# Kernel optimization log

Measured on AMD Instinct MI355X. Metric: run time of the kernel, lower is better.

Reference implementation:

```python
import jax, jax.numpy as jnp
import numpy as np

B, L, D, P = 8, 2048, 1024, 4  # batch, length, word_dim, phrase_len


def setup_inputs() -> dict:
    key = jax.random.key(0)
    kx, kw, kb = jax.random.split(key, 3)
    x = jax.random.normal(kx, (B, L, D), dtype=jnp.float32)
    # torch nn.Linear(phrase_dim, word_dim): W [out=D, in=D*P], b [D]
    scale = 1.0 / np.sqrt(D * P)
    W = jax.random.uniform(kw, (D, D * P), dtype=jnp.float32, minval=-scale, maxval=scale)
    b = jax.random.uniform(kb, (D,), dtype=jnp.float32, minval=-scale, maxval=scale)
    return {"x": x, "W": W, "b": b}


def reference(x, W, b):
    Bs, Ls, Ds = x.shape
    Ps = W.shape[1] // Ds  # phrase_len
    # gram[i][:, t] = x[:, t - i] (zero for t < i): left-pad by i, keep first L steps.
    # Stack on the LAST axis then reshape, matching torch's contiguous view over
    # (dim, phrase_len) -> feature index d*P + i.
    grams = jnp.stack(
        [jnp.pad(x, ((0, 0), (i, 0), (0, 0)))[:, :Ls, :] for i in range(Ps)],
        axis=-1,
    )  # [B, L, D, P]
    feat = grams.reshape(Bs, Ls, Ds * Ps)  # [B, L, D*P]
    # nn.Linear: y = feat @ W.T + b
    return jnp.einsum("blf,df->bld", feat, W) + b
```

## Files before the change

kernel.cpp:

```cpp
#include <hip/hip_runtime.h>
#include <hip/hip_bf16.h>
#include <stdint.h>

#define Bq 8
#define Lq 2048
#define Dq 1024
#define Pq 4
#define Kq 4096
#define LPAD 2056
#define BM 256
#define BN 256
#define BK 64

typedef __attribute__((ext_vector_type(8))) short short8;
typedef __attribute__((ext_vector_type(4))) float f32x4;

__device__ __forceinline__ unsigned short f2bf(float f) {
  unsigned u = __float_as_uint(f);
  u += 0x7FFFu + ((u >> 16) & 1u);
  return (unsigned short)(u >> 16);
}

__device__ __forceinline__ void gload_lds16(const void* g, void* l) {
  __builtin_amdgcn_global_load_lds(
      (const __attribute__((address_space(1))) void*)g,
      (__attribute__((address_space(3))) void*)l, 16, 0, 0);
}

__global__ void k_prep(const float* __restrict__ x, const float* __restrict__ W,
                       unsigned short* __restrict__ xp, unsigned short* __restrict__ Wp) {
  if (blockIdx.x < 8224u) {
    unsigned g = blockIdx.x * blockDim.x + threadIdx.x;
    unsigned base = g * 8;
    const unsigned total = (unsigned)Bq * LPAD * Dq;
    if (base >= total) return;
    unsigned t = base >> 10;
    unsigned b = t / LPAD;
    unsigned r = t - b * LPAD;
    unsigned d = base & 1023;
    short8 o;
    if (r >= 3 && r < 3 + Lq) {
      const float* s = x + ((size_t)b * Lq + (r - 3)) * Dq + d;
      float4 v0 = *(const float4*)(s);
      float4 v1 = *(const float4*)(s + 4);
      o[0] = (short)f2bf(v0.x); o[1] = (short)f2bf(v0.y);
      o[2] = (short)f2bf(v0.z); o[3] = (short)f2bf(v0.w);
      o[4] = (short)f2bf(v1.x); o[5] = (short)f2bf(v1.y);
      o[6] = (short)f2bf(v1.z); o[7] = (short)f2bf(v1.w);
    } else {
      o = (short8)0;
    }
    *(short8*)(xp + base) = o;
  } else {
    unsigned g = (blockIdx.x - 8224u) * blockDim.x + threadIdx.x;
    unsigned base = g * 8;
    unsigned d = base >> 12;
    unsigned rem = base & 4095;
    unsigned dp = rem >> 2;
    const float4* src = (const float4*)(W + base);
    float4 v0 = src[0];
    float4 v1 = src[1];
    float a0[4] = {v0.x, v0.y, v0.z, v0.w};
    float a1[4] = {v1.x, v1.y, v1.z, v1.w};
#pragma unroll
    for (int i = 0; i < 4; ++i) {
      unsigned packed = (unsigned)f2bf(a0[i]) | ((unsigned)f2bf(a1[i]) << 16);
      *(unsigned*)(Wp + (size_t)d * 4096 + (size_t)i * 1024 + dp) = packed;
    }
  }
}


#define VM6 asm volatile("s_waitcnt vmcnt(6)" ::: "memory")
#define VM4 asm volatile("s_waitcnt vmcnt(4)" ::: "memory")
#define VM0 asm volatile("s_waitcnt vmcnt(0)" ::: "memory")
#define NOPS ((void)0)
#define SCHED_RELAX __builtin_amdgcn_sched_barrier(0x106)

#define STAGE_A(buf, kt, h) do { \
    const int i_ = (kt) >> 4; const int d0_ = ((kt) & 15) << 6; \
    _Pragma("unroll") for (int q_ = 0; q_ < 2; ++q_) { \
      const unsigned short* src_ = xp + (((size_t)(aRowBase + q_ * 128 + (h) * 64 - i_)) << 10) + d0_ + clog; \
      gload_lds16(src_, lds + ((buf) << 16) + ((h) << 14) + (q_ << 13) + (tid << 4)); \
    } } while (0)

#define STAGE_B(buf, kt, h) do { \
    _Pragma("unroll") for (int q_ = 0; q_ < 2; ++q_) { \
      const unsigned short* src_ = Wp + (((size_t)(nBase0 + q_ * 128 + (h) * 32)) << 12) + ((kt) << 6) + clog; \
      gload_lds16(src_, lds + ((buf) << 16) + 32768 + ((h) << 14) + (q_ << 13) + (tid << 4)); \
    } } while (0)

#define PHASE(buf, mh, nh, LOADA, LOADB, STAGE_STMT, VM_STMT) do { \
    if (LOADA) { \
      _Pragma("unroll") for (int mi = 0; mi < 4; ++mi) \
      _Pragma("unroll") for (int kk = 0; kk < 2; ++kk) \
        fa[mi][kk] = *(const short8*)(lds + ((buf) << 16) + ((mh) << 14) + aRowByte[mi] + colByte[kk]); \
    } \
    if (LOADB) { \
      _Pragma("unroll") for (int ni = 0; ni < 2; ++ni) \
      _Pragma("unroll") for (int kk = 0; kk < 2; ++kk) \
        fb[ni][kk] = *(const short8*)(lds + ((buf) << 16) + 32768 + ((nh) << 14) + bRowByte[ni] + colByte[kk]); \
    } \
    STAGE_STMT; \
    VM_STMT; \
    __builtin_amdgcn_s_barrier(); \
    SCHED_RELAX; \
    __builtin_amdgcn_s_setprio(1); \
    _Pragma("unroll") for (int mi = 0; mi < 4; ++mi) \
    _Pragma("unroll") for (int ni = 0; ni < 2; ++ni) \
    _Pragma("unroll") for (int kk = 0; kk < 2; ++kk) \
      acc[(mh) * 4 + mi][(nh) * 2 + ni] = __builtin_amdgcn_mfma_f32_16x16x32_bf16( \
          fa[mi][kk], fb[ni][kk], acc[(mh) * 4 + mi][(nh) * 2 + ni], 0, 0, 0); \
    __builtin_amdgcn_s_setprio(0); \
    __builtin_amdgcn_s_barrier(); \
    SCHED_RELAX; \
  } while (0)

__global__ void __launch_bounds__(512, 2)
k_gemm(const unsigned short* __restrict__ xp,
       const unsigned short* __restrict__ Wp,
       const float* __restrict__ bias,
       float* __restrict__ out) {
  __shared__ __attribute__((aligned(16))) unsigned char lds[131072];

  const int tid  = threadIdx.x;
  const int lane = tid & 63;
  const int w    = tid >> 6;
  const int wm   = w >> 2;
  const int wn   = w & 3;

  const int bid = blockIdx.x;
  const int swz = (bid & 7) * 32 + (bid >> 3);
  const int m0 = (swz >> 2) * BM;
  const int n0 = (swz & 3) * BN;
  const int b  = m0 >> 11;
  const int l0 = m0 & 2047;

  const int sr0 = tid >> 3;
  const int clog = ((tid & 7) ^ (sr0 & 7)) << 3;
  const int aRowBase = b * LPAD + l0 + 3 + sr0;
  const int nBase0 = n0 + ((sr0 >> 5) << 6) + (sr0 & 31);

  int aRowByte[4], bRowByte[2], colByte[2];
#pragma unroll
  for (int mi = 0; mi < 4; ++mi) aRowByte[mi] = (wm * 64 + mi * 16 + (lane & 15)) << 7;
#pragma unroll
  for (int ni = 0; ni < 2; ++ni) bRowByte[ni] = (wn * 32 + ni * 16 + (lane & 15)) << 7;
#pragma unroll
  for (int kk = 0; kk < 2; ++kk)
    colByte[kk] = (kk * 64 + ((lane >> 4) << 4)) ^ ((lane & 7) << 4);

  f32x4 acc[8][4] = {};
  short8 fa[4][2], fb[2][2];

  STAGE_A(0, 0, 0);
  STAGE_B(0, 0, 1);
  STAGE_A(0, 0, 1);
  STAGE_B(0, 0, 0);
  VM4;
  STAGE_A(1, 1, 0);
  STAGE_B(1, 1, 1);
  STAGE_A(1, 1, 1);
  VM6;
  __builtin_amdgcn_s_barrier();
  SCHED_RELAX;

#pragma unroll 1
  for (int it = 0; it < 31; ++it) {
    const int kt0 = it * 2;
    PHASE(0, 0, 0, 1, 1, STAGE_B(1, kt0 + 1, 0), NOPS);
    PHASE(0, 0, 1, 0, 1, STAGE_A(0, kt0 + 2, 0), NOPS);
    PHASE(0, 1, 1, 1, 0, STAGE_B(0, kt0 + 2, 1), NOPS);
    PHASE(0, 1, 0, 0, 1, STAGE_A(0, kt0 + 2, 1), VM6);
    PHASE(1, 0, 0, 1, 1, STAGE_B(0, kt0 + 2, 0), NOPS);
    PHASE(1, 0, 1, 0, 1, STAGE_A(1, kt0 + 3, 0), NOPS);
    PHASE(1, 1, 1, 1, 0, STAGE_B(1, kt0 + 3, 1), NOPS);
    PHASE(1, 1, 0, 0, 1, STAGE_A(1, kt0 + 3, 1), VM6);
  }

  PHASE(0, 0, 0, 1, 1, STAGE_B(1, 63, 0), NOPS);
  PHASE(0, 0, 1, 0, 1, NOPS, NOPS);
  PHASE(0, 1, 1, 1, 0, NOPS, NOPS);
  PHASE(0, 1, 0, 0, 1, NOPS, VM0);
  PHASE(1, 0, 0, 1, 1, NOPS, NOPS);
  PHASE(1, 0, 1, 0, 1, NOPS, NOPS);
  PHASE(1, 1, 1, 1, 0, NOPS, NOPS);
  PHASE(1, 1, 0, 0, 1, NOPS, NOPS);

#pragma unroll
  for (int nig = 0; nig < 4; ++nig) {
    const int col = n0 + wn * 64 + nig * 16 + (lane & 15);
    const float bv = bias[col];
#pragma unroll
    for (int mig = 0; mig < 8; ++mig) {
      const int row0 = m0 + wm * 128 + mig * 16 + ((lane >> 4) << 2);
#pragma unroll
      for (int t2 = 0; t2 < 4; ++t2)
        out[(size_t)(row0 + t2) * Dq + col] = acc[mig][nig][t2] + bv;
    }
  }
}

__global__ void k_naive(const float* __restrict__ x, const float* __restrict__ W,
                        const float* __restrict__ bias, float* __restrict__ out) {
  size_t g = (size_t)blockIdx.x * blockDim.x + threadIdx.x;
  const size_t total = (size_t)Bq * Lq * Dq;
  if (g >= total) return;
  int d = (int)(g & 1023);
  int l = (int)((g >> 10) & 2047);
  int b = (int)(g >> 21);
  float s = bias[d];
  for (int i = 0; i < Pq; ++i) {
    if (l - i < 0) continue;
    const float* xr = x + ((size_t)b * Lq + (l - i)) * Dq;
    const float* wr = W + (size_t)d * Kq + i;
    float accv = 0.f;
    for (int dp = 0; dp < Dq; ++dp) accv += xr[dp] * wr[(size_t)dp * 4];
    s += accv;
  }
  out[g] = s;
}

extern "C" void kernel_launch(void* const* d_in, const int* in_sizes, int n_in,
                              void* d_out, int out_size, void* d_ws, size_t ws_size,
                              hipStream_t stream) {
  const float* x    = (const float*)d_in[0];
  const float* W    = (const float*)d_in[1];
  const float* bias = (const float*)d_in[2];
  float* out = (float*)d_out;

  const size_t WP_BYTES = (size_t)Dq * Kq * sizeof(unsigned short);
  const size_t XP_BYTES = (size_t)Bq * LPAD * Dq * sizeof(unsigned short);

  if (ws_size < WP_BYTES + XP_BYTES) {
    const size_t total = (size_t)Bq * Lq * Dq;
    k_naive<<<(unsigned)((total + 255) / 256), 256, 0, stream>>>(x, W, bias, out);
    return;
  }

  unsigned short* Wp = (unsigned short*)d_ws;
  unsigned short* xp = (unsigned short*)((char*)d_ws + WP_BYTES);

  k_prep<<<10272, 256, 0, stream>>>(x, W, xp, Wp);
  k_gemm<<<dim3((Bq * Lq / BM) * (Dq / BN)), 512, 0, stream>>>(xp, Wp, bias, out);
}
```

Measured before the change: 135.6 us.

## Double-buffer register fragments to overlap LDS reads with MFMA in GEMM loop

Replaces the single fa/fb register fragment set with ping-pong sets (aX/aY, bX/bY). The LDS reads for the next quadrant are issued before the current quadrant's MFMAs, using explicit lgkmcnt waits and a sched_barrier that keeps MFMAs from being reordered. The aim is to hide LDS read latency behind matrix math instead of stalling on it after each barrier. The cost is higher register pressure under launch bounds of 512 threads at 2 blocks, and a fragile hand-written barrier and waitcnt schedule.

```diff
diff --git a/kernel.cpp b/kernel.cpp
--- a/kernel.cpp
+++ b/kernel.cpp
@@ -74,8 +74,9 @@
 #define VM6 asm volatile("s_waitcnt vmcnt(6)" ::: "memory")
 #define VM4 asm volatile("s_waitcnt vmcnt(4)" ::: "memory")
 #define VM0 asm volatile("s_waitcnt vmcnt(0)" ::: "memory")
-#define NOPS ((void)0)
-#define SCHED_RELAX __builtin_amdgcn_sched_barrier(0x106)
+#define LGKM(n) asm volatile("s_waitcnt lgkmcnt(" #n ")" ::: "memory")
+#define SB_NOMFMA __builtin_amdgcn_sched_barrier(0x3F7)
+#define BAR __builtin_amdgcn_s_barrier()
 
 #define STAGE_A(buf, kt, h) do { \
     const int i_ = (kt) >> 4; const int d0_ = ((kt) & 15) << 6; \
@@ -90,30 +91,26 @@
       gload_lds16(src_, lds + ((buf) << 16) + 32768 + ((h) << 14) + (q_ << 13) + (tid << 4)); \
     } } while (0)
 
-#define PHASE(buf, mh, nh, LOADA, LOADB, STAGE_STMT, VM_STMT) do { \
-    if (LOADA) { \
-      _Pragma("unroll") for (int mi = 0; mi < 4; ++mi) \
-      _Pragma("unroll") for (int kk = 0; kk < 2; ++kk) \
-        fa[mi][kk] = *(const short8*)(lds + ((buf) << 16) + ((mh) << 14) + aRowByte[mi] + colByte[kk]); \
-    } \
-    if (LOADB) { \
-      _Pragma("unroll") for (int ni = 0; ni < 2; ++ni) \
-      _Pragma("unroll") for (int kk = 0; kk < 2; ++kk) \
-        fb[ni][kk] = *(const short8*)(lds + ((buf) << 16) + 32768 + ((nh) << 14) + bRowByte[ni] + colByte[kk]); \
-    } \
-    STAGE_STMT; \
-    VM_STMT; \
-    __builtin_amdgcn_s_barrier(); \
-    SCHED_RELAX; \
+#define READ_A(dst, buf, h) do { \
+    _Pragma("unroll") for (int mi = 0; mi < 4; ++mi) \
+    _Pragma("unroll") for (int kk = 0; kk < 2; ++kk) \
+      dst[mi][kk] = *(const short8*)(lds + ((buf) << 16) + ((h) << 14) + aRowByte[mi] + colByte[kk]); \
+  } while (0)
+
+#define READ_B(dst, buf, h) do { \
+    _Pragma("unroll") for (int ni = 0; ni < 2; ++ni) \
+    _Pragma("unroll") for (int kk = 0; kk < 2; ++kk) \
+      dst[ni][kk] = *(const short8*)(lds + ((buf) << 16) + 32768 + ((h) << 14) + bRowByte[ni] + colByte[kk]); \
+  } while (0)
+
+#define MFMAQ(mh, nh, A, Bv) do { \
     __builtin_amdgcn_s_setprio(1); \
     _Pragma("unroll") for (int mi = 0; mi < 4; ++mi) \
     _Pragma("unroll") for (int ni = 0; ni < 2; ++ni) \
     _Pragma("unroll") for (int kk = 0; kk < 2; ++kk) \
       acc[(mh) * 4 + mi][(nh) * 2 + ni] = __builtin_amdgcn_mfma_f32_16x16x32_bf16( \
-          fa[mi][kk], fb[ni][kk], acc[(mh) * 4 + mi][(nh) * 2 + ni], 0, 0, 0); \
+          A[mi][kk], Bv[ni][kk], acc[(mh) * 4 + mi][(nh) * 2 + ni], 0, 0, 0); \
     __builtin_amdgcn_s_setprio(0); \
-    __builtin_amdgcn_s_barrier(); \
-    SCHED_RELAX; \
   } while (0)
 
 __global__ void __launch_bounds__(512, 2)
@@ -151,7 +148,7 @@
     colByte[kk] = (kk * 64 + ((lane >> 4) << 4)) ^ ((lane & 7) << 4);
 
   f32x4 acc[8][4] = {};
-  short8 fa[4][2], fb[2][2];
+  short8 aX[4][2], aY[4][2], bX[2][2], bY[2][2];
 
   STAGE_A(0, 0, 0);
   STAGE_B(0, 0, 1);
@@ -162,30 +159,97 @@
   STAGE_B(1, 1, 1);
   STAGE_A(1, 1, 1);
   VM6;
-  __builtin_amdgcn_s_barrier();
-  SCHED_RELAX;
+  BAR;
+  READ_A(aX, 0, 0);
+  READ_B(bX, 0, 0);
 
 #pragma unroll 1
   for (int it = 0; it < 31; ++it) {
-    const int kt0 = it * 2;
-    PHASE(0, 0, 0, 1, 1, STAGE_B(1, kt0 + 1, 0), NOPS);
-    PHASE(0, 0, 1, 0, 1, STAGE_A(0, kt0 + 2, 0), NOPS);
-    PHASE(0, 1, 1, 1, 0, STAGE_B(0, kt0 + 2, 1), NOPS);
-    PHASE(0, 1, 0, 0, 1, STAGE_A(0, kt0 + 2, 1), VM6);
-    PHASE(1, 0, 0, 1, 1, STAGE_B(0, kt0 + 2, 0), NOPS);
-    PHASE(1, 0, 1, 0, 1, STAGE_A(1, kt0 + 3, 0), NOPS);
-    PHASE(1, 1, 1, 1, 0, STAGE_B(1, kt0 + 3, 1), NOPS);
-    PHASE(1, 1, 0, 0, 1, STAGE_A(1, kt0 + 3, 1), VM6);
-  }
-
-  PHASE(0, 0, 0, 1, 1, STAGE_B(1, 63, 0), NOPS);
-  PHASE(0, 0, 1, 0, 1, NOPS, NOPS);
-  PHASE(0, 1, 1, 1, 0, NOPS, NOPS);
-  PHASE(0, 1, 0, 0, 1, NOPS, VM0);
-  PHASE(1, 0, 0, 1, 1, NOPS, NOPS);
-  PHASE(1, 0, 1, 0, 1, NOPS, NOPS);
-  PHASE(1, 1, 1, 1, 0, NOPS, NOPS);
-  PHASE(1, 1, 0, 0, 1, NOPS, NOPS);
+    const int T = it * 2;
+    STAGE_B(1, T + 1, 0);
+    BAR;
+    READ_B(bY, 0, 1);
+    LGKM(4); SB_NOMFMA;
+    MFMAQ(0, 0, aX, bX);
+    BAR;
+    STAGE_A(0, T + 2, 0);
+    BAR;
+    READ_A(aY, 0, 1);
+    LGKM(8); SB_NOMFMA;
+    MFMAQ(0, 1, aX, bY);
+    BAR;
+    STAGE_B(0, T + 2, 1);
+    BAR;
+    LGKM(0); SB_NOMFMA;
+    MFMAQ(1, 1, aY, bY);
+    BAR;
+    STAGE_A(0, T + 2, 1);
+    VM6;
+    BAR;
+    READ_A(aX, 1, 0);
+    READ_B(bY, 1, 0);
+    LGKM(12); SB_NOMFMA;
+    MFMAQ(1, 0, aY, bX);
+    BAR;
+    STAGE_B(0, T + 2, 0);
+    BAR;
+    READ_B(bX, 1, 1);
+    LGKM(4); SB_NOMFMA;
+    MFMAQ(0, 0, aX, bY);
+    BAR;
+    STAGE_A(1, T + 3, 0);
+    BAR;
+    READ_A(aY, 1, 1);
+    LGKM(8); SB_NOMFMA;
+    MFMAQ(0, 1, aX, bX);
+    BAR;
+    STAGE_B(1, T + 3, 1);
+    BAR;
+    LGKM(0); SB_NOMFMA;
+    MFMAQ(1, 1, aY, bX);
+    BAR;
+    STAGE_A(1, T + 3, 1);
+    VM6;
+    BAR;
+    READ_A(aX, 0, 0);
+    READ_B(bX, 0, 0);
+    LGKM(12); SB_NOMFMA;
+    MFMAQ(1, 0, aY, bY);
+    BAR;
+  }
+
+  STAGE_B(1, 63, 0);
+  BAR;
+  READ_B(bY, 0, 1);
+  LGKM(4); SB_NOMFMA;
+  MFMAQ(0, 0, aX, bX);
+  BAR;
+  READ_A(aY, 0, 1);
+  LGKM(8); SB_NOMFMA;
+  MFMAQ(0, 1, aX, bY);
+  BAR;
+  LGKM(0); SB_NOMFMA;
+  MFMAQ(1, 1, aY, bY);
+  BAR;
+  VM0;
+  BAR;
+  READ_A(aX, 1, 0);
+  READ_B(bY, 1, 0);
+  LGKM(12); SB_NOMFMA;
+  MFMAQ(1, 0, aY, bX);
+  BAR;
+  READ_B(bX, 1, 1);
+  LGKM(4); SB_NOMFMA;
+  MFMAQ(0, 0, aX, bY);
+  BAR;
+  READ_A(aY, 1, 1);
+  LGKM(8); SB_NOMFMA;
+  MFMAQ(0, 1, aX, bX);
+  BAR;
+  LGKM(0); SB_NOMFMA;
+  MFMAQ(1, 1, aY, bX);
+  LGKM(0); SB_NOMFMA;
+  MFMAQ(1, 0, aY, bY);
 
 #pragma unroll
   for (int nig = 0; nig < 4; ++nig) {
```

After: 206.6 us. +52.3%, slower.

## Switch GEMM to 4-wave blocks with double-buffered register fragments

Applied to the files above, without the earlier changes.

Changes the GEMM from 8 waves (512 threads) to 4 waves (256 threads) per block. Each wave now computes a 128x128 sub-tile with 8x8 accumulators instead of 128x64. LDS fragment reads are ping-ponged between two register sets (aU/aV, bU/bV), so the next quadrant's reads overlap the current quadrant's MFMAs, with one barrier per phase instead of two. This aims to raise MFMA density and reuse per wave and cut barrier overhead, at the cost of higher register pressure (launch bounds 256,1) and fewer waves to hide latency.

```diff
diff --git a/kernel.cpp b/kernel.cpp
--- a/kernel.cpp
+++ b/kernel.cpp
@@ -71,52 +71,52 @@
 }
 
 
-#define VM6 asm volatile("s_waitcnt vmcnt(6)" ::: "memory")
-#define VM4 asm volatile("s_waitcnt vmcnt(4)" ::: "memory")
-#define VM0 asm volatile("s_waitcnt vmcnt(0)" ::: "memory")
+#define VM16 asm volatile("s_waitcnt vmcnt(16)" ::: "memory")
+#define VM12 asm volatile("s_waitcnt vmcnt(12)" ::: "memory")
+#define VM8  asm volatile("s_waitcnt vmcnt(8)"  ::: "memory")
+#define VM4  asm volatile("s_waitcnt vmcnt(4)"  ::: "memory")
+#define VM0  asm volatile("s_waitcnt vmcnt(0)"  ::: "memory")
+#define BAR  __builtin_amdgcn_s_barrier()
 #define NOPS ((void)0)
-#define SCHED_RELAX __builtin_amdgcn_sched_barrier(0x106)
 
 #define STAGE_A(buf, kt, h) do { \
     const int i_ = (kt) >> 4; const int d0_ = ((kt) & 15) << 6; \
-    _Pragma("unroll") for (int q_ = 0; q_ < 2; ++q_) { \
-      const unsigned short* src_ = xp + (((size_t)(aRowBase + q_ * 128 + (h) * 64 - i_)) << 10) + d0_ + clog; \
-      gload_lds16(src_, lds + ((buf) << 16) + ((h) << 14) + (q_ << 13) + (tid << 4)); \
+    _Pragma("unroll") for (int q_ = 0; q_ < 4; ++q_) { \
+      const unsigned short* src_ = xp + (((size_t)(aRowBase + (q_ >> 1) * 128 + (h) * 64 + (q_ & 1) * 32 - i_)) << 10) + d0_ + clog; \
+      gload_lds16(src_, lds + ((buf) << 16) + ((h) << 14) + (q_ << 12) + (tid << 4)); \
     } } while (0)
 
 #define STAGE_B(buf, kt, h) do { \
-    _Pragma("unroll") for (int q_ = 0; q_ < 2; ++q_) { \
-      const unsigned short* src_ = Wp + (((size_t)(nBase0 + q_ * 128 + (h) * 32)) << 12) + ((kt) << 6) + clog; \
-      gload_lds16(src_, lds + ((buf) << 16) + 32768 + ((h) << 14) + (q_ << 13) + (tid << 4)); \
+    _Pragma("unroll") for (int q_ = 0; q_ < 4; ++q_) { \
+      const unsigned short* src_ = Wp + (((size_t)(nBase0 + (q_ >> 1) * 128 + (h) * 64 + (q_ & 1) * 32)) << 12) + ((kt) << 6) + clog; \
+      gload_lds16(src_, lds + ((buf) << 16) + 32768 + ((h) << 14) + (q_ << 12) + (tid << 4)); \
     } } while (0)
 
-#define PHASE(buf, mh, nh, LOADA, LOADB, STAGE_STMT, VM_STMT) do { \
-    if (LOADA) { \
-      _Pragma("unroll") for (int mi = 0; mi < 4; ++mi) \
-      _Pragma("unroll") for (int kk = 0; kk < 2; ++kk) \
-        fa[mi][kk] = *(const short8*)(lds + ((buf) << 16) + ((mh) << 14) + aRowByte[mi] + colByte[kk]); \
-    } \
-    if (LOADB) { \
-      _Pragma("unroll") for (int ni = 0; ni < 2; ++ni) \
-      _Pragma("unroll") for (int kk = 0; kk < 2; ++kk) \
-        fb[ni][kk] = *(const short8*)(lds + ((buf) << 16) + 32768 + ((nh) << 14) + bRowByte[ni] + colByte[kk]); \
-    } \
-    STAGE_STMT; \
-    VM_STMT; \
-    __builtin_amdgcn_s_barrier(); \
-    SCHED_RELAX; \
-    __builtin_amdgcn_s_setprio(1); \
+#define READ_A(dst, buf, mh) do { \
     _Pragma("unroll") for (int mi = 0; mi < 4; ++mi) \
-    _Pragma("unroll") for (int ni = 0; ni < 2; ++ni) \
     _Pragma("unroll") for (int kk = 0; kk < 2; ++kk) \
-      acc[(mh) * 4 + mi][(nh) * 2 + ni] = __builtin_amdgcn_mfma_f32_16x16x32_bf16( \
-          fa[mi][kk], fb[ni][kk], acc[(mh) * 4 + mi][(nh) * 2 + ni], 0, 0, 0); \
-    __builtin_amdgcn_s_setprio(0); \
-    __builtin_amdgcn_s_barrier(); \
-    SCHED_RELAX; \
-  } while (0)
-
-__global__ void __launch_bounds__(512, 2)
+      dst[mi][kk] = *(const short8*)(lds + ((buf) << 16) + ((mh) << 14) + aRowByte[mi] + colByte[kk]); \
+  } while (0)
+
+#define READ_B(dst, buf, nh) do { \
+    _Pragma("unroll") for (int ni = 0; ni < 4; ++ni) \
+    _Pragma("unroll") for (int kk = 0; kk < 2; ++kk) \
+      dst[ni][kk] = *(const short8*)(lds + ((buf) << 16) + 32768 + ((nh) << 14) + bRowByte[ni] + colByte[kk]); \
+  } while (0)
+
+#define MFMAQ(mh, nh, Aa, Bb) do { \
+    _Pragma("unroll") for (int mi = 0; mi < 4; ++mi) \
+    _Pragma("unroll") for (int ni = 0; ni < 4; ++ni) \
+    _Pragma("unroll") for (int kk = 0; kk < 2; ++kk) \
+      acc[(mh) * 4 + mi][(nh) * 4 + ni] = __builtin_amdgcn_mfma_f32_16x16x32_bf16( \
+          Aa[mi][kk], Bb[ni][kk], acc[(mh) * 4 + mi][(nh) * 4 + ni], 0, 0, 0); \
+  } while (0)
+
+#define PH(RD, ST, VM, mh, nh, Aa, Bb) do { \
+    ST; VM; RD; MFMAQ(mh, nh, Aa, Bb); BAR; \
+  } while (0)
+
+__global__ void __launch_bounds__(256, 1)
 k_gemm(const unsigned short* __restrict__ xp,
        const unsigned short* __restrict__ Wp,
        const float* __restrict__ bias,
@@ -126,8 +126,8 @@
   const int tid  = threadIdx.x;
   const int lane = tid & 63;
   const int w    = tid >> 6;
-  const int wm   = w >> 2;
-  const int wn   = w & 3;
+  const int wm   = w >> 1;
+  const int wn   = w & 1;
 
   const int bid = blockIdx.x;
   const int swz = (bid & 7) * 32 + (bid >> 3);
@@ -139,57 +139,56 @@
   const int sr0 = tid >> 3;
   const int clog = ((tid & 7) ^ (sr0 & 7)) << 3;
   const int aRowBase = b * LPAD + l0 + 3 + sr0;
-  const int nBase0 = n0 + ((sr0 >> 5) << 6) + (sr0 & 31);
-
-  int aRowByte[4], bRowByte[2], colByte[2];
+  const int nBase0 = n0 + sr0;
+
+  int aRowByte[4], bRowByte[4], colByte[2];
 #pragma unroll
   for (int mi = 0; mi < 4; ++mi) aRowByte[mi] = (wm * 64 + mi * 16 + (lane & 15)) << 7;
 #pragma unroll
-  for (int ni = 0; ni < 2; ++ni) bRowByte[ni] = (wn * 32 + ni * 16 + (lane & 15)) << 7;
+  for (int ni = 0; ni < 4; ++ni) bRowByte[ni] = (wn * 64 + ni * 16 + (lane & 15)) << 7;
 #pragma unroll
   for (int kk = 0; kk < 2; ++kk)
     colByte[kk] = (kk * 64 + ((lane >> 4) << 4)) ^ ((lane & 7) << 4);
 
-  f32x4 acc[8][4] = {};
-  short8 fa[4][2], fb[2][2];
+  f32x4 acc[8][8] = {};
+  short8 aU[4][2], aV[4][2], bU[4][2], bV[4][2];
 
   STAGE_A(0, 0, 0);
+  STAGE_B(0, 0, 0);
+  STAGE_A(0, 0, 1);
   STAGE_B(0, 0, 1);
-  STAGE_A(0, 0, 1);
-  STAGE_B(0, 0, 0);
-  VM4;
   STAGE_A(1, 1, 0);
-  STAGE_B(1, 1, 1);
-  STAGE_A(1, 1, 1);
-  VM6;
-  __builtin_amdgcn_s_barrier();
-  SCHED_RELAX;
+  STAGE_B(1, 1, 0);
+  VM16;
+  BAR;
+  READ_A(aU, 0, 0);
+  READ_B(bU, 0, 0);
 
 #pragma unroll 1
   for (int it = 0; it < 31; ++it) {
-    const int kt0 = it * 2;
-    PHASE(0, 0, 0, 1, 1, STAGE_B(1, kt0 + 1, 0), NOPS);
-    PHASE(0, 0, 1, 0, 1, STAGE_A(0, kt0 + 2, 0), NOPS);
-    PHASE(0, 1, 1, 1, 0, STAGE_B(0, kt0 + 2, 1), NOPS);
-    PHASE(0, 1, 0, 0, 1, STAGE_A(0, kt0 + 2, 1), VM6);
-    PHASE(1, 0, 0, 1, 1, STAGE_B(0, kt0 + 2, 0), NOPS);
-    PHASE(1, 0, 1, 0, 1, STAGE_A(1, kt0 + 3, 0), NOPS);
-    PHASE(1, 1, 1, 1, 0, STAGE_B(1, kt0 + 3, 1), NOPS);
-    PHASE(1, 1, 0, 0, 1, STAGE_A(1, kt0 + 3, 1), VM6);
-  }
-
-  PHASE(0, 0, 0, 1, 1, STAGE_B(1, 63, 0), NOPS);
-  PHASE(0, 0, 1, 0, 1, NOPS, NOPS);
-  PHASE(0, 1, 1, 1, 0, NOPS, NOPS);
-  PHASE(0, 1, 0, 0, 1, NOPS, VM0);
-  PHASE(1, 0, 0, 1, 1, NOPS, NOPS);
-  PHASE(1, 0, 1, 0, 1, NOPS, NOPS);
-  PHASE(1, 1, 1, 1, 0, NOPS, NOPS);
-  PHASE(1, 1, 0, 0, 1, NOPS, NOPS);
-
-#pragma unroll
-  for (int nig = 0; nig < 4; ++nig) {
-    const int col = n0 + wn * 64 + nig * 16 + (lane & 15);
+    const int T = it * 2;
+    PH(READ_B(bV, 0, 1), STAGE_B(1, T + 1, 1), VM12, 0, 0, aU, bU);
+    PH(READ_A(aV, 0, 1), STAGE_A(1, T + 1, 1), VM12, 0, 1, aU, bV);
+    PH(READ_A(aU, 1, 0), STAGE_A(0, T + 2, 0), VM12, 1, 1, aV, bV);
+    PH(READ_B(bV, 1, 0), STAGE_B(0, T + 2, 0), VM12, 1, 0, aV, bU);
+    PH(READ_B(bU, 1, 1), STAGE_B(0, T + 2, 1), VM12, 0, 0, aU, bV);
+    PH(READ_A(aV, 1, 1), STAGE_A(0, T + 2, 1), VM12, 0, 1, aU, bU);
+    PH(READ_A(aU, 0, 0), STAGE_A(1, T + 3, 0), VM12, 1, 1, aV, bU);
+    PH(READ_B(bU, 0, 0), STAGE_B(1, T + 3, 0), VM12, 1, 0, aV, bV);
+  }
+
+  PH(READ_B(bV, 0, 1), STAGE_B(1, 63, 1), VM12, 0, 0, aU, bU);
+  PH(READ_A(aV, 0, 1), STAGE_A(1, 63, 1), VM12, 0, 1, aU, bV);
+  PH(READ_A(aU, 1, 0), NOPS,              VM8,  1, 1, aV, bV);
+  PH(READ_B(bV, 1, 0), NOPS,              VM8,  1, 0, aV, bU);
+  PH(READ_B(bU, 1, 1), NOPS,              VM4,  0, 0, aU, bV);
+  PH(READ_A(aV, 1, 1), NOPS,              VM0,  0, 1, aU, bU);
+  PH(NOPS,             NOPS,              NOPS, 1, 1, aV, bU);
+  PH(NOPS,             NOPS,              NOPS, 1, 0, aV, bV);
+
+#pragma unroll
+  for (int nig = 0; nig < 8; ++nig) {
+    const int col = n0 + wn * 128 + nig * 16 + (lane & 15);
     const float bv = bias[col];
 #pragma unroll
     for (int mig = 0; mig < 8; ++mig) {
@@ -242,5 +241,5 @@
   unsigned short* xp = (unsigned short*)((char*)d_ws + WP_BYTES);
 
   k_prep<<<10272, 256, 0, stream>>>(x, W, xp, Wp);
-  k_gemm<<<dim3((Bq * Lq / BM) * (Dq / BN)), 512, 0, stream>>>(xp, Wp, bias, out);
-}
+  k_gemm<<<dim3((Bq * Lq / BM) * (Dq / BN)), 256, 0, stream>>>(xp, Wp, bias, out);
+}
```

After: 208.5 us. 53.7% more time.

## Split GEMM warps into ping-pong groups alternating LDS reads and MFMA

Applied to the files above, without the earlier changes.

Replaces the eight-phase per-K-tile schedule with a two-group ping-pong scheme. The first four warps stage the x tile and the other four stage the W tile. Each group alternates between reading a whole K tile from LDS and running all its MFMAs, offset by one barrier step, so one group computes while the other loads. The LDS layout is reorganised into per-half 32KB buffers, and occupancy is set to one block of 512 threads per CU. The aim is to hide LDS and global-load latency behind matrix-core work. The cost is one resident block per CU and a full vmcnt(0) wait every half-iteration.

```diff
diff --git a/kernel.cpp b/kernel.cpp
--- a/kernel.cpp
+++ b/kernel.cpp
@@ -71,52 +71,60 @@
 }
 
 
-#define VM6 asm volatile("s_waitcnt vmcnt(6)" ::: "memory")
-#define VM4 asm volatile("s_waitcnt vmcnt(4)" ::: "memory")
 #define VM0 asm volatile("s_waitcnt vmcnt(0)" ::: "memory")
-#define NOPS ((void)0)
-#define SCHED_RELAX __builtin_amdgcn_sched_barrier(0x106)
-
-#define STAGE_A(buf, kt, h) do { \
-    const int i_ = (kt) >> 4; const int d0_ = ((kt) & 15) << 6; \
-    _Pragma("unroll") for (int q_ = 0; q_ < 2; ++q_) { \
-      const unsigned short* src_ = xp + (((size_t)(aRowBase + q_ * 128 + (h) * 64 - i_)) << 10) + d0_ + clog; \
-      gload_lds16(src_, lds + ((buf) << 16) + ((h) << 14) + (q_ << 13) + (tid << 4)); \
-    } } while (0)
-
-#define STAGE_B(buf, kt, h) do { \
-    _Pragma("unroll") for (int q_ = 0; q_ < 2; ++q_) { \
-      const unsigned short* src_ = Wp + (((size_t)(nBase0 + q_ * 128 + (h) * 32)) << 12) + ((kt) << 6) + clog; \
-      gload_lds16(src_, lds + ((buf) << 16) + 32768 + ((h) << 14) + (q_ << 13) + (tid << 4)); \
-    } } while (0)
-
-#define PHASE(buf, mh, nh, LOADA, LOADB, STAGE_STMT, VM_STMT) do { \
-    if (LOADA) { \
-      _Pragma("unroll") for (int mi = 0; mi < 4; ++mi) \
-      _Pragma("unroll") for (int kk = 0; kk < 2; ++kk) \
-        fa[mi][kk] = *(const short8*)(lds + ((buf) << 16) + ((mh) << 14) + aRowByte[mi] + colByte[kk]); \
+#define BAR __builtin_amdgcn_s_barrier()
+#define SBF __builtin_amdgcn_sched_barrier(0xF)
+
+#define STAGE_T(buf, kt) do { \
+    if (gE) { \
+      _Pragma("unroll") for (int h_ = 0; h_ < 2; ++h_) \
+      _Pragma("unroll") for (int q_ = 0; q_ < 4; ++q_) { \
+        const unsigned scl_ = (((unsigned)(bRow0 + ((q_ >> 1) * 128 + (q_ & 1) * 32 + h_ * 64) - ((kt) >> 4))) << 11) + (((unsigned)(kt) & 15u) << 7); \
+        gload_lds16((const char*)xp + (thrS + scl_), \
+                    lds + (((buf) << 15) + (h_ << 14) + (q_ << 12)) + (tt << 4)); \
+      } \
+    } else { \
+      _Pragma("unroll") for (int h_ = 0; h_ < 2; ++h_) \
+      _Pragma("unroll") for (int q_ = 0; q_ < 4; ++q_) { \
+        const unsigned scl_ = (((unsigned)(n0 + q_ * 64 + h_ * 32)) << 13) + ((unsigned)(kt) << 7); \
+        gload_lds16((const char*)Wp + (thrS + scl_), \
+                    lds + 65536 + (((buf) << 15) + (h_ << 14) + (q_ << 12)) + (tt << 4)); \
+      } \
     } \
-    if (LOADB) { \
-      _Pragma("unroll") for (int ni = 0; ni < 2; ++ni) \
-      _Pragma("unroll") for (int kk = 0; kk < 2; ++kk) \
-        fb[ni][kk] = *(const short8*)(lds + ((buf) << 16) + 32768 + ((nh) << 14) + bRowByte[ni] + colByte[kk]); \
-    } \
-    STAGE_STMT; \
-    VM_STMT; \
-    __builtin_amdgcn_s_barrier(); \
-    SCHED_RELAX; \
-    __builtin_amdgcn_s_setprio(1); \
+  } while (0)
+
+#define RD_A(dst, buf, h) do { \
+    _Pragma("unroll") for (int mi = 0; mi < 4; ++mi) \
+    _Pragma("unroll") for (int kk = 0; kk < 2; ++kk) \
+      dst[mi][kk] = *(const short8*)(lds + aK[kk] + (((buf) << 15) + ((h) << 14) + (mi << 11))); \
+  } while (0)
+
+#define RD_B(dst, buf, h) do { \
+    _Pragma("unroll") for (int ni = 0; ni < 2; ++ni) \
+    _Pragma("unroll") for (int kk = 0; kk < 2; ++kk) \
+      dst[ni][kk] = *(const short8*)(lds + bK[kk] + (((buf) << 15) + ((h) << 14) + (ni << 11))); \
+  } while (0)
+
+#define READ_TILE(buf) do { \
+    RD_A(fa0, buf, 0); RD_A(fa1, buf, 1); RD_B(bX, buf, 0); RD_B(bY, buf, 1); \
+  } while (0)
+
+#define MFMAH(mh, nh, A, Bv) do { \
+    _Pragma("unroll") for (int kk = 0; kk < 2; ++kk) \
     _Pragma("unroll") for (int mi = 0; mi < 4; ++mi) \
     _Pragma("unroll") for (int ni = 0; ni < 2; ++ni) \
-    _Pragma("unroll") for (int kk = 0; kk < 2; ++kk) \
       acc[(mh) * 4 + mi][(nh) * 2 + ni] = __builtin_amdgcn_mfma_f32_16x16x32_bf16( \
-          fa[mi][kk], fb[ni][kk], acc[(mh) * 4 + mi][(nh) * 2 + ni], 0, 0, 0); \
+          A[mi][kk], Bv[ni][kk], acc[(mh) * 4 + mi][(nh) * 2 + ni], 0, 0, 0); \
+  } while (0)
+
+#define MFMA_TILE() do { \
+    __builtin_amdgcn_s_setprio(1); \
+    MFMAH(0, 0, fa0, bX); MFMAH(0, 1, fa0, bY); \
+    MFMAH(1, 0, fa1, bX); MFMAH(1, 1, fa1, bY); \
     __builtin_amdgcn_s_setprio(0); \
-    __builtin_amdgcn_s_barrier(); \
-    SCHED_RELAX; \
-  } while (0)
-
-__global__ void __launch_bounds__(512, 2)
+  } while (0)
+
+__global__ void __launch_bounds__(512, 1)
 k_gemm(const unsigned short* __restrict__ xp,
        const unsigned short* __restrict__ Wp,
        const float* __restrict__ bias,
@@ -128,6 +136,7 @@
   const int w    = tid >> 6;
   const int wm   = w >> 2;
   const int wn   = w & 3;
+  const bool gE  = (wm == 0);
 
   const int bid = blockIdx.x;
   const int swz = (bid & 7) * 32 + (bid >> 3);
@@ -135,57 +144,57 @@
   const int n0 = (swz & 3) * BN;
   const int b  = m0 >> 11;
   const int l0 = m0 & 2047;
-
-  const int sr0 = tid >> 3;
-  const int clog = ((tid & 7) ^ (sr0 & 7)) << 3;
-  const int aRowBase = b * LPAD + l0 + 3 + sr0;
-  const int nBase0 = n0 + ((sr0 >> 5) << 6) + (sr0 & 31);
-
-  int aRowByte[4], bRowByte[2], colByte[2];
-#pragma unroll
-  for (int mi = 0; mi < 4; ++mi) aRowByte[mi] = (wm * 64 + mi * 16 + (lane & 15)) << 7;
-#pragma unroll
-  for (int ni = 0; ni < 2; ++ni) bRowByte[ni] = (wn * 32 + ni * 16 + (lane & 15)) << 7;
-#pragma unroll
-  for (int kk = 0; kk < 2; ++kk)
-    colByte[kk] = (kk * 64 + ((lane >> 4) << 4)) ^ ((lane & 7) << 4);
+  const int bRow0 = b * LPAD + l0 + 3;
+
+  const int tt = tid & 255;
+  const int sr = tt >> 3;
+  const unsigned clogB = ((unsigned)((tid & 7) ^ (sr & 7))) << 4;
+  const unsigned thrS = gE ? ((((unsigned)sr) << 11) + clogB)
+                           : ((((unsigned)sr) << 13) + clogB);
+
+  unsigned aK[2], bK[2];
+  {
+    const int slot = (lane >> 4) << 4;
+    const int sw = (lane & 7) << 4;
+#pragma unroll
+    for (int kk = 0; kk < 2; ++kk) {
+      const int cb = (kk * 64 + slot) ^ sw;
+      aK[kk] = (unsigned)((wm << 13) + ((lane & 15) << 7) + cb);
+      bK[kk] = (unsigned)(65536 + ((wn * 32 + (lane & 15)) << 7) + cb);
+    }
+  }
 
   f32x4 acc[8][4] = {};
-  short8 fa[4][2], fb[2][2];
-
-  STAGE_A(0, 0, 0);
-  STAGE_B(0, 0, 1);
-  STAGE_A(0, 0, 1);
-  STAGE_B(0, 0, 0);
-  VM4;
-  STAGE_A(1, 1, 0);
-  STAGE_B(1, 1, 1);
-  STAGE_A(1, 1, 1);
-  VM6;
-  __builtin_amdgcn_s_barrier();
-  SCHED_RELAX;
+  short8 fa0[4][2], fa1[4][2], bX[2][2], bY[2][2];
+
+  STAGE_T(0, 0);
+  VM0; BAR; SBF;
+  if (gE) { READ_TILE(0); }
+  STAGE_T(1, 1);
+  BAR; SBF;
+  if (gE) { MFMA_TILE(); } else { READ_TILE(0); }
+  VM0; BAR; SBF;
 
 #pragma unroll 1
   for (int it = 0; it < 31; ++it) {
-    const int kt0 = it * 2;
-    PHASE(0, 0, 0, 1, 1, STAGE_B(1, kt0 + 1, 0), NOPS);
-    PHASE(0, 0, 1, 0, 1, STAGE_A(0, kt0 + 2, 0), NOPS);
-    PHASE(0, 1, 1, 1, 0, STAGE_B(0, kt0 + 2, 1), NOPS);
-    PHASE(0, 1, 0, 0, 1, STAGE_A(0, kt0 + 2, 1), VM6);
-    PHASE(1, 0, 0, 1, 1, STAGE_B(0, kt0 + 2, 0), NOPS);
-    PHASE(1, 0, 1, 0, 1, STAGE_A(1, kt0 + 3, 0), NOPS);
-    PHASE(1, 1, 1, 1, 0, STAGE_B(1, kt0 + 3, 1), NOPS);
-    PHASE(1, 1, 0, 0, 1, STAGE_A(1, kt0 + 3, 1), VM6);
-  }
-
-  PHASE(0, 0, 0, 1, 1, STAGE_B(1, 63, 0), NOPS);
-  PHASE(0, 0, 1, 0, 1, NOPS, NOPS);
-  PHASE(0, 1, 1, 1, 0, NOPS, NOPS);
-  PHASE(0, 1, 0, 0, 1, NOPS, VM0);
-  PHASE(1, 0, 0, 1, 1, NOPS, NOPS);
-  PHASE(1, 0, 1, 0, 1, NOPS, NOPS);
-  PHASE(1, 1, 1, 1, 0, NOPS, NOPS);
-  PHASE(1, 1, 0, 0, 1, NOPS, NOPS);
+    const int V = 2 * it + 2;
+    STAGE_T(0, V);
+    if (gE) { READ_TILE(1); } else { MFMA_TILE(); }
+    BAR; SBF;
+    if (gE) { MFMA_TILE(); } else { READ_TILE(1); }
+    VM0; BAR; SBF;
+    STAGE_T(1, V + 1);
+    if (gE) { READ_TILE(0); } else { MFMA_TILE(); }
+    BAR; SBF;
+    if (gE) { MFMA_TILE(); } else { READ_TILE(0); }
+    VM0; BAR; SBF;
+  }
+
+  if (gE) { READ_TILE(1); } else { MFMA_TILE(); }
+  BAR; SBF;
+  if (gE) { MFMA_TILE(); } else { READ_TILE(1); }
+  BAR; SBF;
+  if (!gE) { MFMA_TILE(); }
 
 #pragma unroll
   for (int nig = 0; nig < 4; ++nig) {
```

Result: slower. 159.5 us (+17.6%).
